# Kernel tuning notes

Hardware: AMD Instinct MI355X
Metric: run time of the kernel (lower is better)

The kernel has to match this reference:

```python
import jax, jax.numpy as jnp
import numpy as np
import math

B, S, H, NH = 4, 2048, 768, 12
HD = H // NH
EPS = 1e-12

def setup_inputs() -> dict:
    key = jax.random.key(0)
    ks = jax.random.split(key, 12)
    sc = 0.02
    return {
        "hidden_states": jax.random.normal(ks[0], (B, S, H), jnp.float32),
        "attention_mask": jnp.zeros((B, 1, 1, S), jnp.float32),
        "Wq": jax.random.normal(ks[1], (H, H), jnp.float32) * sc,
        "bq": jnp.zeros((H,), jnp.float32),
        "Wk": jax.random.normal(ks[2], (H, H), jnp.float32) * sc,
        "bk": jnp.zeros((H,), jnp.float32),
        "Wv": jax.random.normal(ks[3], (H, H), jnp.float32) * sc,
        "bv": jnp.zeros((H,), jnp.float32),
        "Wo": jax.random.normal(ks[4], (H, H), jnp.float32) * sc,
        "bo": jnp.zeros((H,), jnp.float32),
        "ln_g": jnp.ones((H,), jnp.float32),
        "ln_b": jnp.zeros((H,), jnp.float32),
    }

def _heads(x):
    # [B,S,H] -> [B,NH,S,HD]
    return x.reshape(B, S, NH, HD).transpose(0, 2, 1, 3)

def reference(hidden_states, attention_mask, Wq, bq, Wk, bk, Wv, bv, Wo, bo, ln_g, ln_b):
    q = _heads(hidden_states @ Wq.T + bq)
    k = _heads(hidden_states @ Wk.T + bk)
    v = _heads(hidden_states @ Wv.T + bv)
    # eager attention: [B,NH,S,S]
    scores = jnp.einsum("bhqd,bhkd->bhqk", q, k) / math.sqrt(HD)
    scores = scores + attention_mask
    probs = jax.nn.softmax(scores, axis=-1)
    ctx = jnp.einsum("bhqk,bhkd->bhqd", probs, v)
    ctx = ctx.transpose(0, 2, 1, 3).reshape(B, S, H)
    # output dense + residual + LayerNorm (dropout is identity in eval)
    h = ctx @ Wo.T + bo + hidden_states
    mu = jnp.mean(h, axis=-1, keepdims=True)
    var = jnp.mean(jnp.square(h - mu), axis=-1, keepdims=True)
    out = (h - mu) * jax.lax.rsqrt(var + EPS) * ln_g + ln_b
    return out
```

## Files before the change

kernel.cpp:

```cpp
#include <hip/hip_runtime.h>
#include <math.h>

#define B_  4
#define S_  2048
#define H_  768
#define NH_ 12
#define HD_ 64
#define M_  (B_*S_)
#define K_  768
#define LOG2E 1.44269504088896340736f

using bf16x8 = __attribute__((ext_vector_type(8))) short;
using s16x4  = __attribute__((ext_vector_type(4))) short;
using f32x4  = __attribute__((ext_vector_type(4))) float;

__device__ inline short f2bf(float f) {
    union { float f; unsigned u; } v{f};
    unsigned r = (v.u + 0x7FFF + ((v.u >> 16) & 1)) >> 16;
    return (short)r;
}

__device__ inline unsigned cvt_pk_bf16(float lo, float hi) {
    unsigned r;
    asm("v_cvt_pk_bf16_f32 %0, %1, %2" : "=v"(r) : "v"(lo), "v"(hi));
    return r;
}

#define GLDS16(g, l) __builtin_amdgcn_global_load_lds( \
    (const __attribute__((address_space(1))) void*)(g), \
    (__attribute__((address_space(3))) void*)(l), 16, 0, 0)

__device__ inline const bf16x8* LDSRD(const short* base, int row, int colByte) {
    return (const bf16x8*)((const char*)base + ((row << 7) + (colByte ^ ((row & 7) << 4))));
}

__global__ __launch_bounds__(256)
void cvt6(const float* __restrict__ s0, const float* __restrict__ s1,
          const float* __restrict__ s2, const float* __restrict__ s3,
          const float* __restrict__ s4, const float* __restrict__ msk,
          short* __restrict__ d0, short* __restrict__ d1,
          short* __restrict__ d2, short* __restrict__ d3,
          short* __restrict__ d4, float* __restrict__ msk2) {
    const int r = blockIdx.y;
    if (r == 5) {
        for (int i = blockIdx.x * blockDim.x + threadIdx.x; i < (B_ * S_) / 4;
             i += gridDim.x * blockDim.x) {
            float4 v = ((const float4*)msk)[i];
            v.x *= LOG2E; v.y *= LOG2E; v.z *= LOG2E; v.w *= LOG2E;
            ((float4*)msk2)[i] = v;
        }
        return;
    }
    const float* s = r == 0 ? s0 : r == 1 ? s1 : r == 2 ? s2 : r == 3 ? s3 : s4;
    short* d      = r == 0 ? d0 : r == 1 ? d1 : r == 2 ? d2 : r == 3 ? d3 : d4;
    const int n4  = (r == 0 ? M_ * H_ : H_ * H_) >> 2;
    for (int i = blockIdx.x * blockDim.x + threadIdx.x; i < n4; i += gridDim.x * blockDim.x) {
        float4 v = ((const float4*)s)[i];
        s16x4 o;
        o[0] = f2bf(v.x); o[1] = f2bf(v.y); o[2] = f2bf(v.z); o[3] = f2bf(v.w);
        ((s16x4*)d)[i] = o;
    }
}

__global__ __launch_bounds__(256)
void gemm_qkv(const short* __restrict__ A, const short* __restrict__ Bw,
              const float* __restrict__ bq, const float* __restrict__ bk,
              const float* __restrict__ bv, short* __restrict__ obase,
              short* __restrict__ vt) {
    __shared__ __align__(16) short As[128 * 32];
    __shared__ __align__(16) short Bs[128 * 32];
    const int tid = threadIdx.x;
    const int w = tid >> 6, l = tid & 63;
    const int l16 = l & 15, lg = l >> 4;
    const int wm = w >> 1, wn = w & 1;
    const int m0 = blockIdx.x * 128, n0 = blockIdx.y * 128;
    const int which = blockIdx.y / 6;
    const float* bias = which == 0 ? bq : which == 1 ? bk : bv;
    const float scale = which == 0 ? 0.125f * LOG2E : 1.0f;

    f32x4 acc[4][4];
    #pragma unroll
    for (int mi = 0; mi < 4; mi++)
        #pragma unroll
        for (int ni = 0; ni < 4; ni++)
            acc[mi][ni][0] = acc[mi][ni][1] = acc[mi][ni][2] = acc[mi][ni][3] = 0.f;

    for (int k0 = 0; k0 < K_; k0 += 32) {
        #pragma unroll
        for (int i = 0; i < 2; i++) {
            const int o = w * 2048 + i * 1024 + l * 16;
            const int row = o >> 6, colb = o & 63;
            const char* ga = (const char*)A  + (((size_t)(m0 + row)) * K_ + k0) * 2 + colb;
            const char* gb = (const char*)Bw + (((size_t)(n0 + row)) * K_ + k0) * 2 + colb;
            GLDS16(ga, (char*)As + w * 2048 + i * 1024);
            GLDS16(gb, (char*)Bs + w * 2048 + i * 1024);
        }
        __syncthreads();

        bf16x8 af[4], bfr[4];
        #pragma unroll
        for (int mi = 0; mi < 4; mi++)
            af[mi] = *(const bf16x8*)&As[(wm * 64 + mi * 16 + l16) * 32 + lg * 8];
        #pragma unroll
        for (int ni = 0; ni < 4; ni++)
            bfr[ni] = *(const bf16x8*)&Bs[(wn * 64 + ni * 16 + l16) * 32 + lg * 8];
        #pragma unroll
        for (int mi = 0; mi < 4; mi++)
            #pragma unroll
            for (int ni = 0; ni < 4; ni++)
                acc[mi][ni] = __builtin_amdgcn_mfma_f32_16x16x32_bf16(af[mi], bfr[ni], acc[mi][ni], 0, 0, 0);
        __syncthreads();
    }

    const int ncol0 = (blockIdx.y % 6) * 128;
    float bcol[4];
    #pragma unroll
    for (int ni = 0; ni < 4; ni++) bcol[ni] = bias[ncol0 + wn * 64 + ni * 16 + l16];

    const int h = (blockIdx.y % 6) * 2 + wn;
    if (which < 2) {
        short* obf = obase + (size_t)which * M_ * H_;
        #pragma unroll
        for (int mi = 0; mi < 4; mi++) {
            #pragma unroll
            for (int r = 0; r < 4; r++) {
                const int row = m0 + wm * 64 + mi * 16 + lg * 4 + r;
                const int bb = row >> 11, ss = row & 2047;
                const size_t base = (((size_t)(bb * NH_ + h)) * S_ + ss) * HD_;
                #pragma unroll
                for (int ni = 0; ni < 4; ni++)
                    obf[base + ni * 16 + l16] = f2bf((acc[mi][ni][r] + bcol[ni]) * scale);
            }
        }
    } else {
        #pragma unroll
        for (int mi = 0; mi < 4; mi++) {
            const int row0 = m0 + wm * 64 + mi * 16 + lg * 4;
            const int bb = row0 >> 11, ss0 = row0 & 2047;
            #pragma unroll
            for (int ni = 0; ni < 4; ni++) {
                s16x4 pk;
                pk[0] = f2bf(acc[mi][ni][0] + bcol[ni]);
                pk[1] = f2bf(acc[mi][ni][1] + bcol[ni]);
                pk[2] = f2bf(acc[mi][ni][2] + bcol[ni]);
                pk[3] = f2bf(acc[mi][ni][3] + bcol[ni]);
                *(s16x4*)(vt + (((size_t)(bb * NH_ + h)) * HD_ + ni * 16 + l16) * S_ + ss0) = pk;
            }
        }
    }
}

__global__ __launch_bounds__(256)
void gemm_out(const short* __restrict__ A, const short* __restrict__ Bw,
              const float* __restrict__ bias, const float* __restrict__ res,
              float* __restrict__ o) {
    __shared__ __align__(16) short As[128 * 32];
    __shared__ __align__(16) short Bs[128 * 32];
    const int tid = threadIdx.x;
    const int w = tid >> 6, l = tid & 63;
    const int l16 = l & 15, lg = l >> 4;
    const int wm = w >> 1, wn = w & 1;
    const int m0 = blockIdx.x * 128, n0 = blockIdx.y * 128;

    f32x4 acc[4][4];
    #pragma unroll
    for (int mi = 0; mi < 4; mi++)
        #pragma unroll
        for (int ni = 0; ni < 4; ni++)
            acc[mi][ni][0] = acc[mi][ni][1] = acc[mi][ni][2] = acc[mi][ni][3] = 0.f;

    for (int k0 = 0; k0 < K_; k0 += 32) {
        #pragma unroll
        for (int i = 0; i < 2; i++) {
            const int o_ = w * 2048 + i * 1024 + l * 16;
            const int row = o_ >> 6, colb = o_ & 63;
            const char* ga = (const char*)A  + (((size_t)(m0 + row)) * K_ + k0) * 2 + colb;
            const char* gb = (const char*)Bw + (((size_t)(n0 + row)) * K_ + k0) * 2 + colb;
            GLDS16(ga, (char*)As + w * 2048 + i * 1024);
            GLDS16(gb, (char*)Bs + w * 2048 + i * 1024);
        }
        __syncthreads();

        bf16x8 af[4], bfr[4];
        #pragma unroll
        for (int mi = 0; mi < 4; mi++)
            af[mi] = *(const bf16x8*)&As[(wm * 64 + mi * 16 + l16) * 32 + lg * 8];
        #pragma unroll
        for (int ni = 0; ni < 4; ni++)
            bfr[ni] = *(const bf16x8*)&Bs[(wn * 64 + ni * 16 + l16) * 32 + lg * 8];
        #pragma unroll
        for (int mi = 0; mi < 4; mi++)
            #pragma unroll
            for (int ni = 0; ni < 4; ni++)
                acc[mi][ni] = __builtin_amdgcn_mfma_f32_16x16x32_bf16(af[mi], bfr[ni], acc[mi][ni], 0, 0, 0);
        __syncthreads();
    }

    float bcol[4];
    #pragma unroll
    for (int ni = 0; ni < 4; ni++) bcol[ni] = bias[n0 + wn * 64 + ni * 16 + l16];
    #pragma unroll
    for (int mi = 0; mi < 4; mi++) {
        #pragma unroll
        for (int r = 0; r < 4; r++) {
            const int row = m0 + wm * 64 + mi * 16 + lg * 4 + r;
            #pragma unroll
            for (int ni = 0; ni < 4; ni++) {
                const int col = n0 + wn * 64 + ni * 16 + l16;
                o[(size_t)row * H_ + col] = acc[mi][ni][r] + bcol[ni] + res[(size_t)row * H_ + col];
            }
        }
    }
}

__global__ __launch_bounds__(256)
void flash_attn_mfma(const short* __restrict__ q, const short* __restrict__ k,
                     const short* __restrict__ vt, const float* __restrict__ mask,
                     short* __restrict__ ctx) {
    const int qt = blockIdx.x, h = blockIdx.y, b = blockIdx.z;
    __shared__ __align__(16) short KsL[2][4096];
    __shared__ __align__(16) short VtL[2][4096];
    __shared__ __align__(16) short PsL[4096];
    const int tid = threadIdx.x;
    const int w = tid >> 6, l = tid & 63;
    const int l16 = l & 15, lg = l >> 4;

    const size_t bh = (size_t)(b * NH_ + h);
    const size_t qrow = (bh * S_ + qt * 64 + w * 16 + l16) * HD_;
    bf16x8 qf0 = *(const bf16x8*)(q + qrow + lg * 8);
    bf16x8 qf1 = *(const bf16x8*)(q + qrow + 32 + lg * 8);

    const size_t kbase  = bh * S_ * HD_;
    const size_t vtbase = bh * HD_ * S_;

    bf16x8 ones;
    #pragma unroll
    for (int j = 0; j < 8; j++) ones[j] = (short)0x3F80;

    f32x4 oacc[4], lsum;
    #pragma unroll
    for (int i = 0; i < 4; i++) oacc[i][0] = oacc[i][1] = oacc[i][2] = oacc[i][3] = 0.f;
    lsum[0] = lsum[1] = lsum[2] = lsum[3] = 0.f;
    float m_reg = -3.0e38f;

    bf16x8 nk[2], nv[2];
    #define LOADN(ct_) do {                                                       \
        _Pragma("unroll")                                                         \
        for (int i_ = 0; i_ < 2; i_++) {                                          \
            const int c_ = l * 2 + i_;                                            \
            const int row_ = w * 16 + (c_ >> 3);                                  \
            const int cB_ = (c_ & 7) * 16;                                        \
            nk[i_] = *(const bf16x8*)((const char*)(k  + kbase  + (size_t)((ct_) * 64 + row_) * HD_) + cB_); \
            nv[i_] = *(const bf16x8*)((const char*)(vt + vtbase + (size_t)row_ * S_ + (ct_) * 64) + cB_);    \
        }                                                                         \
    } while (0)
    #define WRITEN(bu) do {                                                       \
        _Pragma("unroll")                                                         \
        for (int i_ = 0; i_ < 2; i_++) {                                          \
            const int c_ = l * 2 + i_;                                            \
            const int row_ = w * 16 + (c_ >> 3);                                  \
            const int byte_ = (row_ << 7) + (((c_ & 7) * 16) ^ ((row_ & 7) << 4));\
            *(bf16x8*)((char*)KsL[bu] + byte_) = nk[i_];                          \
            *(bf16x8*)((char*)VtL[bu] + byte_) = nv[i_];                          \
        }                                                                         \
    } while (0)

    LOADN(0);
    WRITEN(0);
    __syncthreads();

    int cbuf = 0;
    for (int ct = 0; ct < S_ / 64; ct++) {
        if (ct + 1 < S_ / 64) LOADN(ct + 1);

        f32x4 sacc[4];
        #pragma unroll
        for (int n = 0; n < 4; n++) {
            float4 mk = *(const float4*)(mask + (size_t)b * S_ + ct * 64 + n * 16 + lg * 4);
            sacc[n][0] = mk.x; sacc[n][1] = mk.y; sacc[n][2] = mk.z; sacc[n][3] = mk.w;
        }
        __builtin_amdgcn_s_setprio(1);
        #pragma unroll
        for (int n = 0; n < 4; n++) {
            bf16x8 kb0 = *LDSRD(KsL[cbuf], n * 16 + l16, lg * 16);
            bf16x8 kb1 = *LDSRD(KsL[cbuf], n * 16 + l16, 64 + lg * 16);
            sacc[n] = __builtin_amdgcn_mfma_f32_16x16x32_bf16(kb0, qf0, sacc[n], 0, 0, 0);
            sacc[n] = __builtin_amdgcn_mfma_f32_16x16x32_bf16(kb1, qf1, sacc[n], 0, 0, 0);
        }
        __builtin_amdgcn_s_setprio(0);

        float x0 = fmaxf(fmaxf(sacc[0][0], sacc[0][1]), fmaxf(sacc[0][2], sacc[0][3]));
        float x1 = fmaxf(fmaxf(sacc[1][0], sacc[1][1]), fmaxf(sacc[1][2], sacc[1][3]));
        float x2 = fmaxf(fmaxf(sacc[2][0], sacc[2][1]), fmaxf(sacc[2][2], sacc[2][3]));
        float x3 = fmaxf(fmaxf(sacc[3][0], sacc[3][1]), fmaxf(sacc[3][2], sacc[3][3]));
        float pmax = fmaxf(fmaxf(x0, x1), fmaxf(x2, x3));
        pmax = fmaxf(pmax, __shfl_xor(pmax, 16));
        pmax = fmaxf(pmax, __shfl_xor(pmax, 32));

        if (!__all(pmax - m_reg <= 8.f)) {
            const float mn = fmaxf(m_reg, pmax);
            const float corr = __builtin_amdgcn_exp2f(m_reg - mn);
            m_reg = mn;
            float corr4[4];
            #pragma unroll
            for (int r = 0; r < 4; r++) corr4[r] = __shfl(corr, lg * 4 + r);
            #pragma unroll
            for (int nd = 0; nd < 4; nd++)
                #pragma unroll
                for (int r = 0; r < 4; r++) oacc[nd][r] *= corr4[r];
            #pragma unroll
            for (int r = 0; r < 4; r++) lsum[r] *= corr4[r];
        }

        const int prow = w * 16 + l16;
        #pragma unroll
        for (int n = 0; n < 4; n++) {
            uint2 pk;
            pk.x = cvt_pk_bf16(__builtin_amdgcn_exp2f(sacc[n][0] - m_reg),
                               __builtin_amdgcn_exp2f(sacc[n][1] - m_reg));
            pk.y = cvt_pk_bf16(__builtin_amdgcn_exp2f(sacc[n][2] - m_reg),
                               __builtin_amdgcn_exp2f(sacc[n][3] - m_reg));
            *(uint2*)((char*)PsL + (prow << 7) + ((32 * n + 8 * lg) ^ ((prow & 7) << 4))) = pk;
        }

        bf16x8 pa0 = *LDSRD(PsL, prow, lg * 16);
        bf16x8 pa1 = *LDSRD(PsL, prow, 64 + lg * 16);
        __builtin_amdgcn_s_setprio(1);
        lsum = __builtin_amdgcn_mfma_f32_16x16x32_bf16(pa0, ones, lsum, 0, 0, 0);
        lsum = __builtin_amdgcn_mfma_f32_16x16x32_bf16(pa1, ones, lsum, 0, 0, 0);
        #pragma unroll
        for (int nd = 0; nd < 4; nd++) {
            bf16x8 vb0 = *LDSRD(VtL[cbuf], nd * 16 + l16, lg * 16);
            bf16x8 vb1 = *LDSRD(VtL[cbuf], nd * 16 + l16, 64 + lg * 16);
            oacc[nd] = __builtin_amdgcn_mfma_f32_16x16x32_bf16(pa0, vb0, oacc[nd], 0, 0, 0);
            oacc[nd] = __builtin_amdgcn_mfma_f32_16x16x32_bf16(pa1, vb1, oacc[nd], 0, 0, 0);
        }
        __builtin_amdgcn_s_setprio(0);

        if (ct + 1 < S_ / 64) WRITEN(cbuf ^ 1);
        __syncthreads();
        cbuf ^= 1;
    }
    #undef LOADN
    #undef WRITEN

    #pragma unroll
    for (int r = 0; r < 4; r++) {
        const float inv = 1.f / lsum[r];
        const size_t row = (size_t)(b * S_ + qt * 64 + w * 16 + lg * 4 + r);
        #pragma unroll
        for (int nd = 0; nd < 4; nd++)
            ctx[row * H_ + h * HD_ + nd * 16 + l16] = f2bf(oacc[nd][r] * inv);
    }
}

__global__ __launch_bounds__(256)
void layernorm_k(const float* __restrict__ hin, const float* __restrict__ g,
                 const float* __restrict__ beta, float* __restrict__ out) {
    const int row = blockIdx.x;
    const int tid = threadIdx.x;
    const float* x = hin + (size_t)row * H_;
    __shared__ float sm[4];

    float v0 = x[tid], v1 = x[tid + 256], v2 = x[tid + 512];
    float s = v0 + v1 + v2;
    #pragma unroll
    for (int o = 32; o > 0; o >>= 1) s += __shfl_xor(s, o);
    if ((tid & 63) == 0) sm[tid >> 6] = s;
    __syncthreads();
    float mu = (sm[0] + sm[1] + sm[2] + sm[3]) * (1.f / 768.f);

    float d0 = v0 - mu, d1 = v1 - mu, d2 = v2 - mu;
    float ss = d0*d0 + d1*d1 + d2*d2;
    #pragma unroll
    for (int o = 32; o > 0; o >>= 1) ss += __shfl_xor(ss, o);
    __syncthreads();
    if ((tid & 63) == 0) sm[tid >> 6] = ss;
    __syncthreads();
    float var = (sm[0] + sm[1] + sm[2] + sm[3]) * (1.f / 768.f);
    float sc = rsqrtf(var + 1e-12f);

    float* y = out + (size_t)row * H_;
    y[tid]       = d0 * sc * g[tid]       + beta[tid];
    y[tid + 256] = d1 * sc * g[tid + 256] + beta[tid + 256];
    y[tid + 512] = d2 * sc * g[tid + 512] + beta[tid + 512];
}

extern "C" void kernel_launch(void* const* d_in, const int* in_sizes, int n_in,
                              void* d_out, int out_size, void* d_ws, size_t ws_size,
                              hipStream_t stream) {
    const float* hs   = (const float*)d_in[0];
    const float* mask = (const float*)d_in[1];
    const float* Wq   = (const float*)d_in[2];
    const float* bq   = (const float*)d_in[3];
    const float* Wk   = (const float*)d_in[4];
    const float* bk   = (const float*)d_in[5];
    const float* Wv   = (const float*)d_in[6];
    const float* bv   = (const float*)d_in[7];
    const float* Wo   = (const float*)d_in[8];
    const float* bo   = (const float*)d_in[9];
    const float* ln_g = (const float*)d_in[10];
    const float* ln_b = (const float*)d_in[11];
    float* out = (float*)d_out;

    const size_t MH = (size_t)M_ * H_;
    const size_t HH = (size_t)H_ * H_;
    short* hsbf = (short*)d_ws;
    short* wqbf = hsbf + MH;
    short* wkbf = wqbf + HH;
    short* wvbf = wkbf + HH;
    short* wobf = wvbf + HH;
    short* qbf  = wobf + HH;
    short* kbf  = qbf + MH;
    short* vtb  = kbf + MH;
    short* cbf  = vtb + MH;
    float* hb   = (float*)(cbf + MH);
    float* msk2 = hb + MH;

    cvt6<<<dim3(256, 6), 256, 0, stream>>>(hs, Wq, Wk, Wv, Wo, mask,
                                           hsbf, wqbf, wkbf, wvbf, wobf, msk2);

    gemm_qkv<<<dim3(M_ / 128, 18), 256, 0, stream>>>(hsbf, wqbf, bq, bk, bv, qbf, vtb);

    flash_attn_mfma<<<dim3(S_ / 64, NH_, B_), 256, 0, stream>>>(qbf, kbf, vtb, msk2, cbf);

    gemm_out<<<dim3(M_ / 128, H_ / 128), 256, 0, stream>>>(cbf, wobf, bo, hs, hb);

    layernorm_k<<<M_, 256, 0, stream>>>(hb, ln_g, ln_b, out);
}
```

Before: 198.1 us.

## Swizzle GEMM block order and unroll flash-attention loop by two with precomputed addresses

Both GEMMs now launch a 1D grid and remap block indices so that groups of 8 M-tiles that share a column tile run close together. This is meant to improve L2 reuse of A and B tiles across concurrently running blocks. The flash-attention loop is unrolled by two with fixed double-buffer indices. LDS and global addresses are precomputed and advanced by pointer increments, which removes per-iteration index arithmetic and the cbuf select at the cost of larger code.

```diff
diff --git a/kernel.cpp b/kernel.cpp
--- a/kernel.cpp
+++ b/kernel.cpp
@@ -29,10 +29,6 @@
 #define GLDS16(g, l) __builtin_amdgcn_global_load_lds( \
     (const __attribute__((address_space(1))) void*)(g), \
     (__attribute__((address_space(3))) void*)(l), 16, 0, 0)
-
-__device__ inline const bf16x8* LDSRD(const short* base, int row, int colByte) {
-    return (const bf16x8*)((const char*)base + ((row << 7) + (colByte ^ ((row & 7) << 4))));
-}
 
 __global__ __launch_bounds__(256)
 void cvt6(const float* __restrict__ s0, const float* __restrict__ s1,
@@ -73,8 +69,12 @@
     const int w = tid >> 6, l = tid & 63;
     const int l16 = l & 15, lg = l >> 4;
     const int wm = w >> 1, wn = w & 1;
-    const int m0 = blockIdx.x * 128, n0 = blockIdx.y * 128;
-    const int which = blockIdx.y / 6;
+    const int flat = blockIdx.x;
+    const int j = flat >> 3;
+    const int mt = (flat & 7) * 8 + (j & 7);
+    const int nty = j >> 3;
+    const int m0 = mt * 128, n0 = nty * 128;
+    const int which = nty / 6;
     const float* bias = which == 0 ? bq : which == 1 ? bk : bv;
     const float scale = which == 0 ? 0.125f * LOG2E : 1.0f;
 
@@ -112,12 +112,12 @@
         __syncthreads();
     }
 
-    const int ncol0 = (blockIdx.y % 6) * 128;
+    const int ncol0 = (nty % 6) * 128;
     float bcol[4];
     #pragma unroll
     for (int ni = 0; ni < 4; ni++) bcol[ni] = bias[ncol0 + wn * 64 + ni * 16 + l16];
 
-    const int h = (blockIdx.y % 6) * 2 + wn;
+    const int h = (nty % 6) * 2 + wn;
     if (which < 2) {
         short* obf = obase + (size_t)which * M_ * H_;
         #pragma unroll
@@ -160,7 +160,10 @@
     const int w = tid >> 6, l = tid & 63;
     const int l16 = l & 15, lg = l >> 4;
     const int wm = w >> 1, wn = w & 1;
-    const int m0 = blockIdx.x * 128, n0 = blockIdx.y * 128;
+    const int flat = blockIdx.x;
+    const int j = flat >> 3;
+    const int m0 = ((flat & 7) * 8 + (j & 7)) * 128;
+    const int n0 = (j >> 3) * 128;
 
     f32x4 acc[4][4];
     #pragma unroll
@@ -230,12 +233,32 @@
     bf16x8 qf0 = *(const bf16x8*)(q + qrow + lg * 8);
     bf16x8 qf1 = *(const bf16x8*)(q + qrow + 32 + lg * 8);
 
-    const size_t kbase  = bh * S_ * HD_;
-    const size_t vtbase = bh * HD_ * S_;
+    const int s_swz = (l16 & 7) << 4;
+    const int aA = l16 * 128 + ((lg * 16) ^ s_swz);
+    const int aB = l16 * 128 + ((64 + lg * 16) ^ s_swz);
+    const int pA = w * 2048 + aA;
+    const int pB = w * 2048 + aB;
+    int pwr[4];
+    #pragma unroll
+    for (int n = 0; n < 4; n++)
+        pwr[n] = w * 2048 + l16 * 128 + ((32 * n + 8 * lg) ^ s_swz);
+    const int wrow = w * 16 + (l >> 2);
+    const int wsz = (wrow & 7) << 4;
+    const int wc0 = ((l * 2) & 7) * 16;
+    const int wr0 = wrow * 128 + (wc0 ^ wsz);
+    const int wr1 = wrow * 128 + ((wc0 + 16) ^ wsz);
+
+    const char* KB = (const char*)KsL;
+    const char* VB = (const char*)VtL;
+    char* PB = (char*)PsL;
+
+    const char* kp = (const char*)(k  + bh * S_ * HD_ + (size_t)wrow * HD_) + wc0;
+    const char* vp = (const char*)(vt + bh * HD_ * S_ + (size_t)wrow * S_) + wc0;
+    const float* mp = mask + (size_t)b * S_ + lg * 4;
 
     bf16x8 ones;
     #pragma unroll
-    for (int j = 0; j < 8; j++) ones[j] = (short)0x3F80;
+    for (int jj = 0; jj < 8; jj++) ones[jj] = (short)0x3F80;
 
     f32x4 oacc[4], lsum;
     #pragma unroll
@@ -243,106 +266,103 @@
     lsum[0] = lsum[1] = lsum[2] = lsum[3] = 0.f;
     float m_reg = -3.0e38f;
 
-    bf16x8 nk[2], nv[2];
-    #define LOADN(ct_) do {                                                       \
+    bf16x8 nk0, nk1, nv0, nv1;
+    #define LOADN() do {                                     \
+        nk0 = *(const bf16x8*)(kp);                          \
+        nk1 = *(const bf16x8*)(kp + 16);                     \
+        nv0 = *(const bf16x8*)(vp);                          \
+        nv1 = *(const bf16x8*)(vp + 16);                     \
+        kp += 64 * HD_ * 2;                                  \
+        vp += 64 * 2;                                        \
+    } while (0)
+    #define WRITEN(bu) do {                                  \
+        *(bf16x8*)((char*)KB + (bu) * 8192 + wr0) = nk0;     \
+        *(bf16x8*)((char*)KB + (bu) * 8192 + wr1) = nk1;     \
+        *(bf16x8*)((char*)VB + (bu) * 8192 + wr0) = nv0;     \
+        *(bf16x8*)((char*)VB + (bu) * 8192 + wr1) = nv1;     \
+    } while (0)
+
+    #define COMPUTE(bu) do {                                                      \
+        f32x4 sacc[4];                                                            \
         _Pragma("unroll")                                                         \
-        for (int i_ = 0; i_ < 2; i_++) {                                          \
-            const int c_ = l * 2 + i_;                                            \
-            const int row_ = w * 16 + (c_ >> 3);                                  \
-            const int cB_ = (c_ & 7) * 16;                                        \
-            nk[i_] = *(const bf16x8*)((const char*)(k  + kbase  + (size_t)((ct_) * 64 + row_) * HD_) + cB_); \
-            nv[i_] = *(const bf16x8*)((const char*)(vt + vtbase + (size_t)row_ * S_ + (ct_) * 64) + cB_);    \
+        for (int n = 0; n < 4; n++) {                                             \
+            float4 mk = *(const float4*)(mp + n * 16);                            \
+            sacc[n][0] = mk.x; sacc[n][1] = mk.y;                                 \
+            sacc[n][2] = mk.z; sacc[n][3] = mk.w;                                 \
         }                                                                         \
+        mp += 64;                                                                 \
+        __builtin_amdgcn_s_setprio(1);                                            \
+        _Pragma("unroll")                                                         \
+        for (int n = 0; n < 4; n++) {                                             \
+            bf16x8 kb0 = *(const bf16x8*)(KB + (bu) * 8192 + n * 2048 + aA);      \
+            bf16x8 kb1 = *(const bf16x8*)(KB + (bu) * 8192 + n * 2048 + aB);      \
+            sacc[n] = __builtin_amdgcn_mfma_f32_16x16x32_bf16(kb0, qf0, sacc[n], 0, 0, 0); \
+            sacc[n] = __builtin_amdgcn_mfma_f32_16x16x32_bf16(kb1, qf1, sacc[n], 0, 0, 0); \
+        }                                                                         \
+        __builtin_amdgcn_s_setprio(0);                                            \
+        float x0 = fmaxf(fmaxf(sacc[0][0], sacc[0][1]), fmaxf(sacc[0][2], sacc[0][3])); \
+        float x1 = fmaxf(fmaxf(sacc[1][0], sacc[1][1]), fmaxf(sacc[1][2], sacc[1][3])); \
+        float x2 = fmaxf(fmaxf(sacc[2][0], sacc[2][1]), fmaxf(sacc[2][2], sacc[2][3])); \
+        float x3 = fmaxf(fmaxf(sacc[3][0], sacc[3][1]), fmaxf(sacc[3][2], sacc[3][3])); \
+        float pmax = fmaxf(fmaxf(x0, x1), fmaxf(x2, x3));                         \
+        pmax = fmaxf(pmax, __shfl_xor(pmax, 16));                                 \
+        pmax = fmaxf(pmax, __shfl_xor(pmax, 32));                                 \
+        if (!__all(pmax - m_reg <= 8.f)) {                                        \
+            const float mn = fmaxf(m_reg, pmax);                                  \
+            const float corr = __builtin_amdgcn_exp2f(m_reg - mn);                \
+            m_reg = mn;                                                           \
+            float corr4[4];                                                       \
+            _Pragma("unroll")                                                     \
+            for (int r = 0; r < 4; r++) corr4[r] = __shfl(corr, lg * 4 + r);      \
+            _Pragma("unroll")                                                     \
+            for (int nd = 0; nd < 4; nd++)                                        \
+                _Pragma("unroll")                                                 \
+                for (int r = 0; r < 4; r++) oacc[nd][r] *= corr4[r];              \
+            _Pragma("unroll")                                                     \
+            for (int r = 0; r < 4; r++) lsum[r] *= corr4[r];                      \
+        }                                                                         \
+        _Pragma("unroll")                                                         \
+        for (int n = 0; n < 4; n++) {                                             \
+            uint2 pk;                                                             \
+            pk.x = cvt_pk_bf16(__builtin_amdgcn_exp2f(sacc[n][0] - m_reg),        \
+                               __builtin_amdgcn_exp2f(sacc[n][1] - m_reg));       \
+            pk.y = cvt_pk_bf16(__builtin_amdgcn_exp2f(sacc[n][2] - m_reg),        \
+                               __builtin_amdgcn_exp2f(sacc[n][3] - m_reg));       \
+            *(uint2*)(PB + pwr[n]) = pk;                                          \
+        }                                                                         \
+        bf16x8 pa0 = *(const bf16x8*)(PB + pA);                                   \
+        bf16x8 pa1 = *(const bf16x8*)(PB + pB);                                   \
+        __builtin_amdgcn_s_setprio(1);                                            \
+        lsum = __builtin_amdgcn_mfma_f32_16x16x32_bf16(pa0, ones, lsum, 0, 0, 0); \
+        lsum = __builtin_amdgcn_mfma_f32_16x16x32_bf16(pa1, ones, lsum, 0, 0, 0); \
+        _Pragma("unroll")                                                         \
+        for (int nd = 0; nd < 4; nd++) {                                          \
+            bf16x8 vb0 = *(const bf16x8*)(VB + (bu) * 8192 + nd * 2048 + aA);     \
+            bf16x8 vb1 = *(const bf16x8*)(VB + (bu) * 8192 + nd * 2048 + aB);     \
+            oacc[nd] = __builtin_amdgcn_mfma_f32_16x16x32_bf16(pa0, vb0, oacc[nd], 0, 0, 0); \
+            oacc[nd] = __builtin_amdgcn_mfma_f32_16x16x32_bf16(pa1, vb1, oacc[nd], 0, 0, 0); \
+        }                                                                         \
+        __builtin_amdgcn_s_setprio(0);                                            \
     } while (0)
-    #define WRITEN(bu) do {                                                       \
-        _Pragma("unroll")                                                         \
-        for (int i_ = 0; i_ < 2; i_++) {                                          \
-            const int c_ = l * 2 + i_;                                            \
-            const int row_ = w * 16 + (c_ >> 3);                                  \
-            const int byte_ = (row_ << 7) + (((c_ & 7) * 16) ^ ((row_ & 7) << 4));\
-            *(bf16x8*)((char*)KsL[bu] + byte_) = nk[i_];                          \
-            *(bf16x8*)((char*)VtL[bu] + byte_) = nv[i_];                          \
-        }                                                                         \
-    } while (0)
-
-    LOADN(0);
+
+    LOADN();
     WRITEN(0);
     __syncthreads();
 
-    int cbuf = 0;
-    for (int ct = 0; ct < S_ / 64; ct++) {
-        if (ct + 1 < S_ / 64) LOADN(ct + 1);
-
-        f32x4 sacc[4];
-        #pragma unroll
-        for (int n = 0; n < 4; n++) {
-            float4 mk = *(const float4*)(mask + (size_t)b * S_ + ct * 64 + n * 16 + lg * 4);
-            sacc[n][0] = mk.x; sacc[n][1] = mk.y; sacc[n][2] = mk.z; sacc[n][3] = mk.w;
-        }
-        __builtin_amdgcn_s_setprio(1);
-        #pragma unroll
-        for (int n = 0; n < 4; n++) {
-            bf16x8 kb0 = *LDSRD(KsL[cbuf], n * 16 + l16, lg * 16);
-            bf16x8 kb1 = *LDSRD(KsL[cbuf], n * 16 + l16, 64 + lg * 16);
-            sacc[n] = __builtin_amdgcn_mfma_f32_16x16x32_bf16(kb0, qf0, sacc[n], 0, 0, 0);
-            sacc[n] = __builtin_amdgcn_mfma_f32_16x16x32_bf16(kb1, qf1, sacc[n], 0, 0, 0);
-        }
-        __builtin_amdgcn_s_setprio(0);
-
-        float x0 = fmaxf(fmaxf(sacc[0][0], sacc[0][1]), fmaxf(sacc[0][2], sacc[0][3]));
-        float x1 = fmaxf(fmaxf(sacc[1][0], sacc[1][1]), fmaxf(sacc[1][2], sacc[1][3]));
-        float x2 = fmaxf(fmaxf(sacc[2][0], sacc[2][1]), fmaxf(sacc[2][2], sacc[2][3]));
-        float x3 = fmaxf(fmaxf(sacc[3][0], sacc[3][1]), fmaxf(sacc[3][2], sacc[3][3]));
-        float pmax = fmaxf(fmaxf(x0, x1), fmaxf(x2, x3));
-        pmax = fmaxf(pmax, __shfl_xor(pmax, 16));
-        pmax = fmaxf(pmax, __shfl_xor(pmax, 32));
-
-        if (!__all(pmax - m_reg <= 8.f)) {
-            const float mn = fmaxf(m_reg, pmax);
-            const float corr = __builtin_amdgcn_exp2f(m_reg - mn);
-            m_reg = mn;
-            float corr4[4];
-            #pragma unroll
-            for (int r = 0; r < 4; r++) corr4[r] = __shfl(corr, lg * 4 + r);
-            #pragma unroll
-            for (int nd = 0; nd < 4; nd++)
-                #pragma unroll
-                for (int r = 0; r < 4; r++) oacc[nd][r] *= corr4[r];
-            #pragma unroll
-            for (int r = 0; r < 4; r++) lsum[r] *= corr4[r];
-        }
-
-        const int prow = w * 16 + l16;
-        #pragma unroll
-        for (int n = 0; n < 4; n++) {
-            uint2 pk;
-            pk.x = cvt_pk_bf16(__builtin_amdgcn_exp2f(sacc[n][0] - m_reg),
-                               __builtin_amdgcn_exp2f(sacc[n][1] - m_reg));
-            pk.y = cvt_pk_bf16(__builtin_amdgcn_exp2f(sacc[n][2] - m_reg),
-                               __builtin_amdgcn_exp2f(sacc[n][3] - m_reg));
-            *(uint2*)((char*)PsL + (prow << 7) + ((32 * n + 8 * lg) ^ ((prow & 7) << 4))) = pk;
-        }
-
-        bf16x8 pa0 = *LDSRD(PsL, prow, lg * 16);
-        bf16x8 pa1 = *LDSRD(PsL, prow, 64 + lg * 16);
-        __builtin_amdgcn_s_setprio(1);
-        lsum = __builtin_amdgcn_mfma_f32_16x16x32_bf16(pa0, ones, lsum, 0, 0, 0);
-        lsum = __builtin_amdgcn_mfma_f32_16x16x32_bf16(pa1, ones, lsum, 0, 0, 0);
-        #pragma unroll
-        for (int nd = 0; nd < 4; nd++) {
-            bf16x8 vb0 = *LDSRD(VtL[cbuf], nd * 16 + l16, lg * 16);
-            bf16x8 vb1 = *LDSRD(VtL[cbuf], nd * 16 + l16, 64 + lg * 16);
-            oacc[nd] = __builtin_amdgcn_mfma_f32_16x16x32_bf16(pa0, vb0, oacc[nd], 0, 0, 0);
-            oacc[nd] = __builtin_amdgcn_mfma_f32_16x16x32_bf16(pa1, vb1, oacc[nd], 0, 0, 0);
-        }
-        __builtin_amdgcn_s_setprio(0);
-
-        if (ct + 1 < S_ / 64) WRITEN(cbuf ^ 1);
-        __syncthreads();
-        cbuf ^= 1;
+    #pragma unroll 1
+    for (int ct = 0; ct < S_ / 64; ct += 2) {
+        LOADN();
+        COMPUTE(0);
+        WRITEN(1);
+        __syncthreads();
+        if (ct + 2 < S_ / 64) LOADN();
+        COMPUTE(1);
+        if (ct + 2 < S_ / 64) WRITEN(0);
+        __syncthreads();
     }
     #undef LOADN
     #undef WRITEN
+    #undef COMPUTE
 
     #pragma unroll
     for (int r = 0; r < 4; r++) {
@@ -420,11 +440,11 @@
     cvt6<<<dim3(256, 6), 256, 0, stream>>>(hs, Wq, Wk, Wv, Wo, mask,
                                            hsbf, wqbf, wkbf, wvbf, wobf, msk2);
 
-    gemm_qkv<<<dim3(M_ / 128, 18), 256, 0, stream>>>(hsbf, wqbf, bq, bk, bv, qbf, vtb);
+    gemm_qkv<<<dim3(1152), 256, 0, stream>>>(hsbf, wqbf, bq, bk, bv, qbf, vtb);
 
     flash_attn_mfma<<<dim3(S_ / 64, NH_, B_), 256, 0, stream>>>(qbf, kbf, vtb, msk2, cbf);
 
-    gemm_out<<<dim3(M_ / 128, H_ / 128), 256, 0, stream>>>(cbf, wobf, bo, hs, hb);
+    gemm_out<<<dim3(384), 256, 0, stream>>>(cbf, wobf, bo, hs, hb);
 
     layernorm_k<<<M_, 256, 0, stream>>>(hb, ln_g, ln_b, out);
 }
```

After: 198.3 us. No clear change (+0.1%).

## Enlarge attention query tile to 128 rows and remap GEMM block order

Applied to the files above, without the earlier changes.

The flash attention kernel now runs 512 threads per block with 128 query rows, so each K/V tile staged in LDS is shared by twice as many queries. Each thread now loads one 16-byte chunk of K and of V per tile instead of two, and the P buffer is doubled. The QKV and output GEMMs now use a flattened 1D grid with a swizzled mapping from block index to tile, grouping M tiles so that tiles running together reuse operands in cache. The trade-off is higher LDS and register use per attention block, which may lower occupancy, and half as many attention blocks.

```diff
diff --git a/kernel.cpp b/kernel.cpp
--- a/kernel.cpp
+++ b/kernel.cpp
@@ -73,8 +73,12 @@
     const int w = tid >> 6, l = tid & 63;
     const int l16 = l & 15, lg = l >> 4;
     const int wm = w >> 1, wn = w & 1;
-    const int m0 = blockIdx.x * 128, n0 = blockIdx.y * 128;
-    const int which = blockIdx.y / 6;
+    const int flat = blockIdx.x;
+    const int j = flat >> 3;
+    const int mt = (flat & 7) * 8 + (j & 7);
+    const int nty = j >> 3;
+    const int m0 = mt * 128, n0 = nty * 128;
+    const int which = nty / 6;
     const float* bias = which == 0 ? bq : which == 1 ? bk : bv;
     const float scale = which == 0 ? 0.125f * LOG2E : 1.0f;
 
@@ -112,12 +116,12 @@
         __syncthreads();
     }
 
-    const int ncol0 = (blockIdx.y % 6) * 128;
+    const int ncol0 = (nty % 6) * 128;
     float bcol[4];
     #pragma unroll
     for (int ni = 0; ni < 4; ni++) bcol[ni] = bias[ncol0 + wn * 64 + ni * 16 + l16];
 
-    const int h = (blockIdx.y % 6) * 2 + wn;
+    const int h = (nty % 6) * 2 + wn;
     if (which < 2) {
         short* obf = obase + (size_t)which * M_ * H_;
         #pragma unroll
@@ -160,7 +164,10 @@
     const int w = tid >> 6, l = tid & 63;
     const int l16 = l & 15, lg = l >> 4;
     const int wm = w >> 1, wn = w & 1;
-    const int m0 = blockIdx.x * 128, n0 = blockIdx.y * 128;
+    const int flat = blockIdx.x;
+    const int j = flat >> 3;
+    const int m0 = ((flat & 7) * 8 + (j & 7)) * 128;
+    const int n0 = (j >> 3) * 128;
 
     f32x4 acc[4][4];
     #pragma unroll
@@ -213,29 +220,31 @@
     }
 }
 
-__global__ __launch_bounds__(256)
+__global__ __launch_bounds__(512)
 void flash_attn_mfma(const short* __restrict__ q, const short* __restrict__ k,
                      const short* __restrict__ vt, const float* __restrict__ mask,
                      short* __restrict__ ctx) {
     const int qt = blockIdx.x, h = blockIdx.y, b = blockIdx.z;
     __shared__ __align__(16) short KsL[2][4096];
     __shared__ __align__(16) short VtL[2][4096];
-    __shared__ __align__(16) short PsL[4096];
+    __shared__ __align__(16) short PsL[8192];
     const int tid = threadIdx.x;
     const int w = tid >> 6, l = tid & 63;
     const int l16 = l & 15, lg = l >> 4;
 
     const size_t bh = (size_t)(b * NH_ + h);
-    const size_t qrow = (bh * S_ + qt * 64 + w * 16 + l16) * HD_;
-    bf16x8 qf0 = *(const bf16x8*)(q + qrow + lg * 8);
-    bf16x8 qf1 = *(const bf16x8*)(q + qrow + 32 + lg * 8);
-
+    bf16x8 qf0, qf1;
+    {
+        const size_t qr = (bh * S_ + (size_t)qt * 128 + w * 16 + l16) * HD_;
+        qf0 = *(const bf16x8*)(q + qr + lg * 8);
+        qf1 = *(const bf16x8*)(q + qr + 32 + lg * 8);
+    }
     const size_t kbase  = bh * S_ * HD_;
     const size_t vtbase = bh * HD_ * S_;
 
     bf16x8 ones;
     #pragma unroll
-    for (int j = 0; j < 8; j++) ones[j] = (short)0x3F80;
+    for (int jj = 0; jj < 8; jj++) ones[jj] = (short)0x3F80;
 
     f32x4 oacc[4], lsum;
     #pragma unroll
@@ -243,35 +252,28 @@
     lsum[0] = lsum[1] = lsum[2] = lsum[3] = 0.f;
     float m_reg = -3.0e38f;
 
-    bf16x8 nk[2], nv[2];
-    #define LOADN(ct_) do {                                                       \
-        _Pragma("unroll")                                                         \
-        for (int i_ = 0; i_ < 2; i_++) {                                          \
-            const int c_ = l * 2 + i_;                                            \
-            const int row_ = w * 16 + (c_ >> 3);                                  \
-            const int cB_ = (c_ & 7) * 16;                                        \
-            nk[i_] = *(const bf16x8*)((const char*)(k  + kbase  + (size_t)((ct_) * 64 + row_) * HD_) + cB_); \
-            nv[i_] = *(const bf16x8*)((const char*)(vt + vtbase + (size_t)row_ * S_ + (ct_) * 64) + cB_);    \
-        }                                                                         \
+    const int srow = tid >> 3;
+    const int sc0  = (tid & 7) * 16;
+    const int wr0  = (srow << 7) + (sc0 ^ ((srow & 7) << 4));
+    const int prow = w * 16 + l16;
+
+    bf16x8 nk, nv;
+    #define LOADT(ct_) do {                                                        \
+        nk = *(const bf16x8*)((const char*)(k  + kbase  + (size_t)((ct_) * 64 + srow) * HD_) + sc0); \
+        nv = *(const bf16x8*)((const char*)(vt + vtbase + (size_t)srow * S_ + (ct_) * 64) + sc0);    \
     } while (0)
-    #define WRITEN(bu) do {                                                       \
-        _Pragma("unroll")                                                         \
-        for (int i_ = 0; i_ < 2; i_++) {                                          \
-            const int c_ = l * 2 + i_;                                            \
-            const int row_ = w * 16 + (c_ >> 3);                                  \
-            const int byte_ = (row_ << 7) + (((c_ & 7) * 16) ^ ((row_ & 7) << 4));\
-            *(bf16x8*)((char*)KsL[bu] + byte_) = nk[i_];                          \
-            *(bf16x8*)((char*)VtL[bu] + byte_) = nv[i_];                          \
-        }                                                                         \
+    #define WRITET(bu_) do {                                                       \
+        *(bf16x8*)((char*)KsL[bu_] + wr0) = nk;                                    \
+        *(bf16x8*)((char*)VtL[bu_] + wr0) = nv;                                    \
     } while (0)
 
-    LOADN(0);
-    WRITEN(0);
+    LOADT(0);
+    WRITET(0);
     __syncthreads();
 
     int cbuf = 0;
     for (int ct = 0; ct < S_ / 64; ct++) {
-        if (ct + 1 < S_ / 64) LOADN(ct + 1);
+        if (ct + 1 < S_ / 64) LOADT(ct + 1);
 
         f32x4 sacc[4];
         #pragma unroll
@@ -312,7 +314,6 @@
             for (int r = 0; r < 4; r++) lsum[r] *= corr4[r];
         }
 
-        const int prow = w * 16 + l16;
         #pragma unroll
         for (int n = 0; n < 4; n++) {
             uint2 pk;
@@ -337,17 +338,17 @@
         }
         __builtin_amdgcn_s_setprio(0);
 
-        if (ct + 1 < S_ / 64) WRITEN(cbuf ^ 1);
+        if (ct + 1 < S_ / 64) WRITET(cbuf ^ 1);
         __syncthreads();
         cbuf ^= 1;
     }
-    #undef LOADN
-    #undef WRITEN
+    #undef LOADT
+    #undef WRITET
 
     #pragma unroll
     for (int r = 0; r < 4; r++) {
         const float inv = 1.f / lsum[r];
-        const size_t row = (size_t)(b * S_ + qt * 64 + w * 16 + lg * 4 + r);
+        const size_t row = (size_t)(b * S_ + qt * 128 + w * 16 + lg * 4 + r);
         #pragma unroll
         for (int nd = 0; nd < 4; nd++)
             ctx[row * H_ + h * HD_ + nd * 16 + l16] = f2bf(oacc[nd][r] * inv);
@@ -420,11 +421,11 @@
     cvt6<<<dim3(256, 6), 256, 0, stream>>>(hs, Wq, Wk, Wv, Wo, mask,
                                            hsbf, wqbf, wkbf, wvbf, wobf, msk2);
 
-    gemm_qkv<<<dim3(M_ / 128, 18), 256, 0, stream>>>(hsbf, wqbf, bq, bk, bv, qbf, vtb);
-
-    flash_attn_mfma<<<dim3(S_ / 64, NH_, B_), 256, 0, stream>>>(qbf, kbf, vtb, msk2, cbf);
-
-    gemm_out<<<dim3(M_ / 128, H_ / 128), 256, 0, stream>>>(cbf, wobf, bo, hs, hb);
+    gemm_qkv<<<dim3(1152), 256, 0, stream>>>(hsbf, wqbf, bq, bk, bv, qbf, vtb);
+
+    flash_attn_mfma<<<dim3(S_ / 128, NH_, B_), 512, 0, stream>>>(qbf, kbf, vtb, msk2, cbf);
+
+    gemm_out<<<dim3(384), 256, 0, stream>>>(cbf, wobf, bo, hs, hb);
 
     layernorm_k<<<M_, 256, 0, stream>>>(hb, ln_g, ln_b, out);
 }
```

Result: faster. 188.3 us (-5.0%).
